# Kernel optimization log

Measured on AMD Instinct MI355X. Metric: run time of the kernel, lower is better.

## Reference

```python
import jax, jax.numpy as jnp
import numpy as np

D = 64            # number of devices (leaves hold D/8 each)
B = 65536         # batch of states
FEAT = 5 + 4 * D  # 261
HID = 128


def setup_inputs() -> dict:
    key = jax.random.key(0)
    ks = jax.random.split(key, 10)
    def nrm(k, shape, s=0.1):
        return jax.random.normal(k, shape, jnp.float32) * s
    return {
        "x": jax.random.normal(ks[0], (B, FEAT), jnp.float32),
        # gate params per depth d: 2^d nodes, weight dim 5 + 4*D/2^d
        "w0": nrm(ks[1], (1, 5 + 4 * D)),
        "b0": jnp.zeros((1,), jnp.float32),
        "w1": nrm(ks[2], (2, 5 + 4 * (D // 2))),
        "b1": jnp.zeros((2,), jnp.float32),
        "w2": nrm(ks[3], (4, 5 + 4 * (D // 4))),
        "b2": jnp.zeros((4,), jnp.float32),
        # leaf prob_dist (torch inits to zeros; random here for a non-trivial baseline)
        "leaf_probs": nrm(ks[4], (8, D // 8), 1.0),
        # critic MLP
        "Wc1": nrm(ks[5], (FEAT, HID)),
        "bc1": jnp.zeros((HID,), jnp.float32),
        "Wc2": nrm(ks[6], (HID, 1)),
        "bc2": jnp.zeros((1,), jnp.float32),
    }


def reference(x, w0, b0, w1, b1, w2, b2, leaf_probs, Wc1, bc1, Wc2, bc2):
    # Batched deterministic ClusterTree routing (exploration disabled).
    x5 = x[:, :5]                       # (B, 5) global features
    dev = x[:, 5:].reshape(B, D, 4)     # (B, D, 4) per-device features
    node = jnp.zeros((B,), jnp.int32)   # current node index at each depth
    cum = jnp.ones((B,), x.dtype)       # product of gate values along path
    for d, (wd, bd) in enumerate([(w0, b0), (w1, b1), (w2, b2)]):
        nd = D >> d                     # devices per node at this depth
        off = node * nd                 # contiguous-cluster start offset
        idx = off[:, None] + jnp.arange(nd)                     # (B, nd)
        dslice = jnp.take_along_axis(dev, idx[:, :, None], 1)   # (B, nd, 4)
        w = wd[node]                    # (B, 5 + 4*nd)
        gate = (jnp.sum(x5 * w[:, :5], -1)
                + jnp.sum(dslice.reshape(B, -1) * w[:, 5:], -1)
                + bd[node])
        val = jax.nn.sigmoid(gate)
        cum = cum * val                 # torch: val * child_output, recursively
        node = node * 2 + (val >= 0.5).astype(jnp.int32)
    p = cum[:, None] * leaf_probs[node]                 # (B, D//8)
    v = jax.nn.relu(x @ Wc1 + bc1) @ Wc2 + bc2          # (B, 1) critic
    return p, v
```

## Files before the change

### kernel.cpp

```cpp
#include <hip/hip_runtime.h>
#include <hip/hip_bf16.h>
#include <stdint.h>

#define NB    65536
#define FEATN 261
#define HIDN  128
#define NSTEP 17
#define SROW  296

#define ROWSG 128
#define NTHR  512

typedef __attribute__((ext_vector_type(8)))  short bf16x8;
typedef __attribute__((ext_vector_type(16))) float f32x16;
typedef float f32x4u __attribute__((ext_vector_type(4), aligned(4)));

#define MFMA32(A, B, C) __builtin_amdgcn_mfma_f32_32x32x16_bf16(A, B, C, 0, 0, 0)

__device__ __forceinline__ uint16_t f2b(float v) {
    __hip_bfloat16 b = __float2bfloat16(v);
    return *reinterpret_cast<uint16_t*>(&b);
}

__global__ void prep_B(const float* __restrict__ Wc1, uint16_t* __restrict__ wsB) {
    int t = blockIdx.x * blockDim.x + threadIdx.x;
    if (t >= NSTEP * 4 * 64) return;
    int p = t >> 6, l = t & 63;
    int s = p >> 2, nt = p & 3;
    int n = nt * 32 + (l & 31);
    int kb = 16 * s + 8 * (l >> 5);
    uint16_t hw[8];
    #pragma unroll
    for (int j = 0; j < 8; ++j) {
        int k = kb + j;
        float v = (k < FEATN) ? Wc1[(size_t)k * HIDN + n] : 0.f;
        hw[j] = f2b(v);
    }
    *reinterpret_cast<uint4*>(wsB + (size_t)p * 512 + l * 8) =
        *reinterpret_cast<uint4*>(hw);
}

__global__ __launch_bounds__(NTHR) void ac_merged(
    const float* __restrict__ x,
    const float* __restrict__ w0, const float* __restrict__ b0,
    const float* __restrict__ w1, const float* __restrict__ b1,
    const float* __restrict__ w2, const float* __restrict__ b2,
    const float* __restrict__ leaf,
    const uint16_t* __restrict__ wsB,
    const float* __restrict__ bc1, const float* __restrict__ Wc2,
    const float* __restrict__ bc2,
    float* __restrict__ out_p, float* __restrict__ out_v)
{
    __shared__ uint16_t Axs[ROWSG * SROW];
    __shared__ float bc1s[HIDN];
    __shared__ float wc2s[HIDN];
    __shared__ float vpart[ROWSG * 2];

    const int tid = threadIdx.x;
    const int g   = blockIdx.x / 5;
    const int r   = blockIdx.x - 5 * g;

    if (r == 0) {
        const int rowBase = g * ROWSG;

        if (tid < HIDN) { bc1s[tid] = bc1[tid]; wc2s[tid] = Wc2[tid]; }
        if (tid < ROWSG) {
            uint16_t* rp = Axs + tid * SROW;
            rp[261] = 0;
            *reinterpret_cast<uint32_t*>(rp + 262) = 0u;
            uint4 z; z.x = z.y = z.z = z.w = 0u;
            *reinterpret_cast<uint4*>(rp + 264) = z;
            *reinterpret_cast<uint4*>(rp + 272) = z;
            *reinterpret_cast<uint4*>(rp + 280) = z;
            *reinterpret_cast<uint4*>(rp + 288) = z;
        }

        {
            int row = tid / 66;
            int seg = tid - row * 66;
            #pragma unroll
            for (int it = 0; it < 17; ++it) {
                const int idx = tid + 512 * it;
                if (idx < ROWSG * 66) {
                    const float* src = x + (size_t)(rowBase + row) * FEATN + 4 * seg;
                    uint16_t* dst = Axs + row * SROW + 4 * seg;
                    if (seg < 65) {
                        f32x4u v = *reinterpret_cast<const f32x4u*>(src);
                        uint32_t p0 = (uint32_t)f2b(v[0]) | ((uint32_t)f2b(v[1]) << 16);
                        uint32_t p1 = (uint32_t)f2b(v[2]) | ((uint32_t)f2b(v[3]) << 16);
                        uint2 pk; pk.x = p0; pk.y = p1;
                        *reinterpret_cast<uint2*>(dst) = pk;
                    } else {
                        dst[0] = f2b(src[0]);
                    }
                }
                row += 7; seg += 50;
                if (seg >= 66) { seg -= 66; row += 1; }
            }
        }
        __syncthreads();

        const int lane = tid & 63;
        const int w    = tid >> 6;
        const int mt   = w >> 1;
        const int nh   = w & 1;

        const uint16_t* arow = Axs + (mt * 32 + (lane & 31)) * SROW + (lane >> 5) * 8;
        const uint16_t* bgl  = wsB + (size_t)(2 * nh) * 512 + lane * 8;

        bf16x8 af[NSTEP], bf0[NSTEP], bf1[NSTEP];
        #pragma unroll
        for (int s = 0; s < NSTEP; ++s) {
            af[s]  = *reinterpret_cast<const bf16x8*>(arow + s * 16);
            bf0[s] = *reinterpret_cast<const bf16x8*>(bgl + (size_t)(s * 4)     * 512);
            bf1[s] = *reinterpret_cast<const bf16x8*>(bgl + (size_t)(s * 4 + 1) * 512);
        }

        f32x16 acc0 = {}, acc1 = {};
        #pragma unroll
        for (int s = 0; s < NSTEP; ++s) {
            acc0 = MFMA32(af[s], bf0[s], acc0);
            acc1 = MFMA32(af[s], bf1[s], acc1);
        }

        {
            const int c = lane & 31;
            const int q = lane >> 5;
            const int n0 = 2 * nh * 32 + c;
            const int n1 = n0 + 32;
            const float bb0 = bc1s[n0], ww0 = wc2s[n0];
            const float bb1 = bc1s[n1], ww1 = wc2s[n1];

            float pv[16];
            #pragma unroll
            for (int reg = 0; reg < 16; ++reg) {
                float h0 = acc0[reg] + bb0; h0 = h0 > 0.f ? h0 : 0.f;
                float h1 = acc1[reg] + bb1; h1 = h1 > 0.f ? h1 : 0.f;
                float t = h0 * ww0 + h1 * ww1;
                t += __shfl_xor(t, 1);
                t += __shfl_xor(t, 2);
                t += __shfl_xor(t, 4);
                t += __shfl_xor(t, 8);
                t += __shfl_xor(t, 16);
                pv[reg] = t;
            }
            #pragma unroll
            for (int reg = 0; reg < 16; ++reg) {
                if (c == reg) {
                    int row_local = (reg & 3) + 8 * (reg >> 2) + 4 * q;
                    vpart[(mt * 32 + row_local) * 2 + nh] = pv[reg];
                }
            }
        }
        __syncthreads();
        if (tid < ROWSG)
            out_v[rowBase + tid] = vpart[tid * 2] + vpart[tid * 2 + 1] + bc2[0];

    } else {
        const int s   = tid & 15;
        const int row = g * ROWSG + (r - 1) * 32 + (tid >> 4);
        const float* xr = x + (size_t)row * FEATN;

        f32x4u w0q[4];
        #pragma unroll
        for (int j = 0; j < 4; ++j)
            w0q[j] = *reinterpret_cast<const f32x4u*>(w0 + 4 * s + 64 * j);
        const float w0t = (s < 5) ? w0[256 + s] : 0.f;

        f32x4u w1aq[2], w1bq[2];
        #pragma unroll
        for (int j = 0; j < 2; ++j) {
            w1aq[j] = *reinterpret_cast<const f32x4u*>(w1 + 5 + 8 * s + 4 * j);
            w1bq[j] = *reinterpret_cast<const f32x4u*>(w1 + 133 + 5 + 8 * s + 4 * j);
        }
        const float w1a5 = (s < 5) ? w1[s]       : 0.f;
        const float w1b5 = (s < 5) ? w1[133 + s] : 0.f;

        f32x4u w2q0 = *reinterpret_cast<const f32x4u*>(w2 + 0 * 69 + 5 + 4 * s);
        f32x4u w2q1 = *reinterpret_cast<const f32x4u*>(w2 + 1 * 69 + 5 + 4 * s);
        f32x4u w2q2 = *reinterpret_cast<const f32x4u*>(w2 + 2 * 69 + 5 + 4 * s);
        f32x4u w2q3 = *reinterpret_cast<const f32x4u*>(w2 + 3 * 69 + 5 + 4 * s);
        float w25_0 = (s < 5) ? w2[0 * 69 + s] : 0.f;
        float w25_1 = (s < 5) ? w2[1 * 69 + s] : 0.f;
        float w25_2 = (s < 5) ? w2[2 * 69 + s] : 0.f;
        float w25_3 = (s < 5) ? w2[3 * 69 + s] : 0.f;

        f32x4u xq[4];
        #pragma unroll
        for (int j = 0; j < 4; ++j)
            xq[j] = *reinterpret_cast<const f32x4u*>(xr + 4 * s + 64 * j);
        const float xt  = (s < 5) ? xr[256 + s] : 0.f;
        const float xs5 = (s < 5) ? xr[s]       : 0.f;

        float part = xt * w0t;
        #pragma unroll
        for (int j = 0; j < 4; ++j)
            #pragma unroll
            for (int c = 0; c < 4; ++c)
                part += xq[j][c] * w0q[j][c];
        part += __shfl_xor(part, 1);
        part += __shfl_xor(part, 2);
        part += __shfl_xor(part, 4);
        part += __shfl_xor(part, 8);
        float gate = part + b0[0];
        int node = (gate >= 0.f) ? 1 : 0;
        float cum = 1.f / (1.f + __expf(-gate));

        {
            const float* base = xr + 5 + 128 * node + 8 * s;
            f32x4u xw0 = *reinterpret_cast<const f32x4u*>(base);
            f32x4u xw1 = *reinterpret_cast<const f32x4u*>(base + 4);
            part = xs5 * (node ? w1b5 : w1a5);
            #pragma unroll
            for (int c = 0; c < 4; ++c) {
                part += xw0[c] * (node ? w1bq[0][c] : w1aq[0][c]);
                part += xw1[c] * (node ? w1bq[1][c] : w1aq[1][c]);
            }
            part += __shfl_xor(part, 1);
            part += __shfl_xor(part, 2);
            part += __shfl_xor(part, 4);
            part += __shfl_xor(part, 8);
            gate = part + b1[node];
            cum *= 1.f / (1.f + __expf(-gate));
            node = node * 2 + ((gate >= 0.f) ? 1 : 0);
        }
        {
            f32x4u xv2 = *reinterpret_cast<const f32x4u*>(xr + 5 + 64 * node + 4 * s);
            f32x4u t0 = (node & 1) ? w2q1 : w2q0;
            f32x4u t1 = (node & 1) ? w2q3 : w2q2;
            f32x4u wsel = (node & 2) ? t1 : t0;
            float w5a = (node & 1) ? w25_1 : w25_0;
            float w5b = (node & 1) ? w25_3 : w25_2;
            float w5sel = (node & 2) ? w5b : w5a;
            part = xs5 * w5sel;
            #pragma unroll
            for (int c = 0; c < 4; ++c) part += xv2[c] * wsel[c];
            part += __shfl_xor(part, 1);
            part += __shfl_xor(part, 2);
            part += __shfl_xor(part, 4);
            part += __shfl_xor(part, 8);
            gate = part + b2[node];
            cum *= 1.f / (1.f + __expf(-gate));
            node = node * 2 + ((gate >= 0.f) ? 1 : 0);
        }
        if (s < 8)
            out_p[(size_t)row * 8 + s] = cum * leaf[node * 8 + s];
    }
}

extern "C" void kernel_launch(void* const* d_in, const int* in_sizes, int n_in,
                              void* d_out, int out_size, void* d_ws, size_t ws_size,
                              hipStream_t stream) {
    const float* x    = (const float*)d_in[0];
    const float* w0   = (const float*)d_in[1];
    const float* b0   = (const float*)d_in[2];
    const float* w1   = (const float*)d_in[3];
    const float* b1   = (const float*)d_in[4];
    const float* w2   = (const float*)d_in[5];
    const float* b2   = (const float*)d_in[6];
    const float* leaf = (const float*)d_in[7];
    const float* Wc1  = (const float*)d_in[8];
    const float* bc1  = (const float*)d_in[9];
    const float* Wc2  = (const float*)d_in[10];
    const float* bc2  = (const float*)d_in[11];

    uint16_t* wsB = (uint16_t*)d_ws;

    float* out_p = (float*)d_out;
    float* out_v = out_p + (size_t)NB * 8;

    prep_B<<<(NSTEP * 4 * 64 + 255) / 256, 256, 0, stream>>>(Wc1, wsB);
    ac_merged<<<(NB / ROWSG) * 5, NTHR, 0, stream>>>(
        x, w0, b0, w1, b1, w2, b2, leaf, wsB, bc1, Wc2, bc2, out_p, out_v);
}
```

Before: 147.4 us.

## Load critic MFMA A-fragments directly from global and halve block size

The critic GEMM no longer stages the 128-row x tile into LDS as bf16. Each lane instead loads its fp32 fragment straight from global memory, converts it to bf16 in registers, and masks the K tail. Blocks shrink from 128 rows and 512 threads to 64 rows and 256 threads, with the tree-routing blocks handling 16 rows each. This removes the LDS footprint, the zero padding, the staging copy and one barrier, which should allow more resident blocks. In exchange the A loads are strided across rows, and the tail step reads a few floats past each row end, including past the end of the buffer for the last row.

```diff
diff --git a/kernel.cpp b/kernel.cpp
--- a/kernel.cpp
+++ b/kernel.cpp
@@ -6,10 +6,7 @@
 #define FEATN 261
 #define HIDN  128
 #define NSTEP 17
-#define SROW  296
-
-#define ROWSG 128
-#define NTHR  512
+#define NTHR  256
 
 typedef __attribute__((ext_vector_type(8)))  short bf16x8;
 typedef __attribute__((ext_vector_type(16))) float f32x16;
@@ -20,6 +17,9 @@
 __device__ __forceinline__ uint16_t f2b(float v) {
     __hip_bfloat16 b = __float2bfloat16(v);
     return *reinterpret_cast<uint16_t*>(&b);
+}
+__device__ __forceinline__ uint32_t pk2(float a, float b) {
+    return (uint32_t)f2b(a) | ((uint32_t)f2b(b) << 16);
 }
 
 __global__ void prep_B(const float* __restrict__ Wc1, uint16_t* __restrict__ wsB) {
@@ -51,85 +51,55 @@
     const float* __restrict__ bc2,
     float* __restrict__ out_p, float* __restrict__ out_v)
 {
-    __shared__ uint16_t Axs[ROWSG * SROW];
-    __shared__ float bc1s[HIDN];
-    __shared__ float wc2s[HIDN];
-    __shared__ float vpart[ROWSG * 2];
+    __shared__ float vpart[64 * 2];
 
     const int tid = threadIdx.x;
     const int g   = blockIdx.x / 5;
     const int r   = blockIdx.x - 5 * g;
 
     if (r == 0) {
-        const int rowBase = g * ROWSG;
-
-        if (tid < HIDN) { bc1s[tid] = bc1[tid]; wc2s[tid] = Wc2[tid]; }
-        if (tid < ROWSG) {
-            uint16_t* rp = Axs + tid * SROW;
-            rp[261] = 0;
-            *reinterpret_cast<uint32_t*>(rp + 262) = 0u;
-            uint4 z; z.x = z.y = z.z = z.w = 0u;
-            *reinterpret_cast<uint4*>(rp + 264) = z;
-            *reinterpret_cast<uint4*>(rp + 272) = z;
-            *reinterpret_cast<uint4*>(rp + 280) = z;
-            *reinterpret_cast<uint4*>(rp + 288) = z;
-        }
-
-        {
-            int row = tid / 66;
-            int seg = tid - row * 66;
-            #pragma unroll
-            for (int it = 0; it < 17; ++it) {
-                const int idx = tid + 512 * it;
-                if (idx < ROWSG * 66) {
-                    const float* src = x + (size_t)(rowBase + row) * FEATN + 4 * seg;
-                    uint16_t* dst = Axs + row * SROW + 4 * seg;
-                    if (seg < 65) {
-                        f32x4u v = *reinterpret_cast<const f32x4u*>(src);
-                        uint32_t p0 = (uint32_t)f2b(v[0]) | ((uint32_t)f2b(v[1]) << 16);
-                        uint32_t p1 = (uint32_t)f2b(v[2]) | ((uint32_t)f2b(v[3]) << 16);
-                        uint2 pk; pk.x = p0; pk.y = p1;
-                        *reinterpret_cast<uint2*>(dst) = pk;
-                    } else {
-                        dst[0] = f2b(src[0]);
-                    }
-                }
-                row += 7; seg += 50;
-                if (seg >= 66) { seg -= 66; row += 1; }
-            }
-        }
-        __syncthreads();
-
+        const int rowBase = g * 64;
         const int lane = tid & 63;
         const int w    = tid >> 6;
         const int mt   = w >> 1;
         const int nh   = w & 1;
-
-        const uint16_t* arow = Axs + (mt * 32 + (lane & 31)) * SROW + (lane >> 5) * 8;
-        const uint16_t* bgl  = wsB + (size_t)(2 * nh) * 512 + lane * 8;
-
-        bf16x8 af[NSTEP], bf0[NSTEP], bf1[NSTEP];
+        const int q    = lane >> 5;
+
+        const float* arow = x + (size_t)(rowBase + mt * 32 + (lane & 31)) * FEATN
+                          + (q << 3);
+        const uint16_t* bgl = wsB + (size_t)(2 * nh) * 512 + lane * 8;
+
+        f32x16 acc0 = {}, acc1 = {};
         #pragma unroll
         for (int s = 0; s < NSTEP; ++s) {
-            af[s]  = *reinterpret_cast<const bf16x8*>(arow + s * 16);
-            bf0[s] = *reinterpret_cast<const bf16x8*>(bgl + (size_t)(s * 4)     * 512);
-            bf1[s] = *reinterpret_cast<const bf16x8*>(bgl + (size_t)(s * 4 + 1) * 512);
-        }
-
-        f32x16 acc0 = {}, acc1 = {};
-        #pragma unroll
-        for (int s = 0; s < NSTEP; ++s) {
-            acc0 = MFMA32(af[s], bf0[s], acc0);
-            acc1 = MFMA32(af[s], bf1[s], acc1);
+            f32x4u lo = *reinterpret_cast<const f32x4u*>(arow + 16 * s);
+            f32x4u hi = *reinterpret_cast<const f32x4u*>(arow + 16 * s + 4);
+            if (s == 16) {
+                const int kb = 256 + (q << 3);
+                #pragma unroll
+                for (int j = 0; j < 4; ++j) {
+                    if (kb + j     >= FEATN) lo[j] = 0.f;
+                    if (kb + 4 + j >= FEATN) hi[j] = 0.f;
+                }
+            }
+            union { bf16x8 v; uint32_t u[4]; } a;
+            a.u[0] = pk2(lo[0], lo[1]);
+            a.u[1] = pk2(lo[2], lo[3]);
+            a.u[2] = pk2(hi[0], hi[1]);
+            a.u[3] = pk2(hi[2], hi[3]);
+
+            bf16x8 b0v = *reinterpret_cast<const bf16x8*>(bgl + (size_t)(s * 4)     * 512);
+            bf16x8 b1v = *reinterpret_cast<const bf16x8*>(bgl + (size_t)(s * 4 + 1) * 512);
+            acc0 = MFMA32(a.v, b0v, acc0);
+            acc1 = MFMA32(a.v, b1v, acc1);
         }
 
         {
-            const int c = lane & 31;
-            const int q = lane >> 5;
+            const int c  = lane & 31;
             const int n0 = 2 * nh * 32 + c;
             const int n1 = n0 + 32;
-            const float bb0 = bc1s[n0], ww0 = wc2s[n0];
-            const float bb1 = bc1s[n1], ww1 = wc2s[n1];
+            const float bb0 = bc1[n0], ww0 = Wc2[n0];
+            const float bb1 = bc1[n1], ww1 = Wc2[n1];
 
             float pv[16];
             #pragma unroll
@@ -153,12 +123,12 @@
             }
         }
         __syncthreads();
-        if (tid < ROWSG)
+        if (tid < 64)
             out_v[rowBase + tid] = vpart[tid * 2] + vpart[tid * 2 + 1] + bc2[0];
 
     } else {
         const int s   = tid & 15;
-        const int row = g * ROWSG + (r - 1) * 32 + (tid >> 4);
+        const int row = g * 64 + (r - 1) * 16 + (tid >> 4);
         const float* xr = x + (size_t)row * FEATN;
 
         f32x4u w0q[4];
@@ -270,6 +240,6 @@
     float* out_v = out_p + (size_t)NB * 8;
 
     prep_B<<<(NSTEP * 4 * 64 + 255) / 256, 256, 0, stream>>>(Wc1, wsB);
-    ac_merged<<<(NB / ROWSG) * 5, NTHR, 0, stream>>>(
+    ac_merged<<<(NB / 64) * 5, NTHR, 0, stream>>>(
         x, w0, b0, w1, b1, w2, b2, leaf, wsB, bc1, Wc2, bc2, out_p, out_v);
 }
```

Result: faster. 143.7 us (-2.6%).
